# Kernel optimization log

Measured on AMD Instinct MI355X. Metric: run time of the kernel, lower is better.

The kernel has to match this reference:

```python
import jax, jax.numpy as jnp
import numpy as np

NUM_GRAPHS = 256
NEG_SLOPE = 0.2


def _gatv2(x, src, dst, Wl, Wr, att, bias, num_nodes):
    # GATv2Conv (heads=1): e_ij = att . leaky_relu(Wl x_j + Wr x_i), softmax over in-edges of i
    xl = x @ Wl  # [N, H] source transform
    xr = x @ Wr  # [N, H] target transform
    msg = xl[src]                      # [E, H]
    e = jax.nn.leaky_relu(msg + xr[dst], NEG_SLOPE) @ att  # [E]
    # segment softmax over destination node
    e_max = jax.ops.segment_max(e, dst, num_segments=num_nodes)
    e_exp = jnp.exp(e - e_max[dst])
    denom = jax.ops.segment_sum(e_exp, dst, num_segments=num_nodes)
    alpha = e_exp / denom[dst]         # [E]
    out = jax.ops.segment_sum(alpha[:, None] * msg, dst, num_segments=num_nodes)
    return out + bias


def setup_inputs() -> dict:
    key = jax.random.key(0)
    ks = jax.random.split(key, 16)
    N, E, D, H, O = 100000, 1600000, 64, 64, 64
    s = 0.05
    inp = {
        "x": jax.random.normal(ks[0], (N, D), dtype=jnp.float32),
        "edge_index": jax.random.randint(ks[1], (2, E), 0, N, dtype=jnp.int64),
        "batch": jnp.sort(jax.random.randint(ks[2], (N,), 0, NUM_GRAPHS, dtype=jnp.int64)),
        "W1l": jax.random.normal(ks[3], (D, H), dtype=jnp.float32) * s,
        "W1r": jax.random.normal(ks[4], (D, H), dtype=jnp.float32) * s,
        "att1": jax.random.normal(ks[5], (H,), dtype=jnp.float32) * s,
        "b1": jnp.zeros((H,), dtype=jnp.float32),
        "W2": jax.random.normal(ks[6], (H, H), dtype=jnp.float32) * s,
        "att2": jax.random.normal(ks[7], (H,), dtype=jnp.float32) * s,
        "b2": jnp.zeros((H,), dtype=jnp.float32),
        "W3": jax.random.normal(ks[8], (H, H), dtype=jnp.float32) * s,
        "att3": jax.random.normal(ks[9], (H,), dtype=jnp.float32) * s,
        "b3": jnp.zeros((H,), dtype=jnp.float32),
        "Wlin": jax.random.normal(ks[10], (H, O), dtype=jnp.float32) * s,
        "blin": jnp.zeros((O,), dtype=jnp.float32),
    }
    return inp


def reference(x, edge_index, batch, W1l, W1r, att1, b1, W2, att2, b2, W3, att3, b3, Wlin, blin):
    N = x.shape[0]
    # PyG GATv2Conv default add_self_loops=True
    loops = jnp.arange(N, dtype=edge_index.dtype)
    src = jnp.concatenate([edge_index[0], loops])
    dst = jnp.concatenate([edge_index[1], loops])

    h = jax.nn.relu(_gatv2(x, src, dst, W1l, W1r, att1, b1, N))
    h = jax.nn.relu(_gatv2(h, src, dst, W2, W2, att2, b2, N))  # share_weights=True
    h = _gatv2(h, src, dst, W3, W3, att3, b3, N)

    # global mean pool over graphs
    sums = jax.ops.segment_sum(h, batch, num_segments=NUM_GRAPHS)
    cnts = jax.ops.segment_sum(jnp.ones((N,), dtype=h.dtype), batch, num_segments=NUM_GRAPHS)
    pooled = sums / jnp.maximum(cnts, 1.0)[:, None]
    # dropout is identity in eval mode
    return pooled @ Wlin + blin
```

## Files before the change

### kernel.cpp

```cpp
#include <hip/hip_runtime.h>
#include <hip/hip_fp16.h>
#include <math.h>

#define NEG_SLOPE 0.2f
#define NUM_GRAPHS 256
#define LOG2E_F 1.44269504088896f

#define EPB   6656
#define EPT   13
#define BCAP  5120
#define MAXB  392

typedef _Float16 half8 __attribute__((ext_vector_type(8)));
typedef _Float16 f16x2 __attribute__((ext_vector_type(2)));
typedef float f32x4 __attribute__((ext_vector_type(4)));
typedef unsigned u32x4 __attribute__((ext_vector_type(4)));

__device__ __forceinline__ half8 bch8(uint4 u) { return __builtin_bit_cast(half8, u); }
__device__ __forceinline__ f16x2 bc2(unsigned u) { return __builtin_bit_cast(f16x2, u); }

__device__ __forceinline__ float hsum8_bcast(float x) {
    x += __int_as_float(__builtin_amdgcn_update_dpp(0, __float_as_int(x), 0x111, 0xF, 0xF, false));
    x += __int_as_float(__builtin_amdgcn_update_dpp(0, __float_as_int(x), 0x112, 0xF, 0xF, false));
    x += __int_as_float(__builtin_amdgcn_update_dpp(0, __float_as_int(x), 0x114, 0xF, 0xF, false));
    return __int_as_float(__builtin_amdgcn_ds_swizzle(__float_as_int(x), 0xF8));
}


__device__ __forceinline__ void bucketA_body(char* smem, int bid, int t,
                                             const int* __restrict__ src,
                                             const int* __restrict__ dst,
                                             unsigned* __restrict__ bucketFill,
                                             uint2* __restrict__ bucketArr,
                                             int E, int NBUCK) {
    uint2* sEdge = (uint2*)smem;
    unsigned* hist  = (unsigned*)(smem + EPB * 8);
    unsigned* lscan = hist + MAXB;
    unsigned* ebase = lscan + MAXB;
    unsigned* efill = ebase + MAXB;
    int e0 = bid * EPB;
    int cntE = E - e0; if (cntE > EPB) cntE = EPB;

    for (int b = t; b < MAXB; b += 512) { hist[b] = 0u; efill[b] = 0u; }
    __syncthreads();

    int es[EPT], ed[EPT];
#pragma unroll
    for (int k = 0; k < EPT; ++k) {
        int i = t + k * 512;
        bool v = i < cntE;
        es[k] = v ? src[e0 + i] : 0;
        ed[k] = v ? dst[e0 + i] : -1;
        if (v) atomicAdd(&hist[(unsigned)ed[k] >> 8], 1u);
    }
    __syncthreads();

    if (t < 64) {
        unsigned vals[7]; unsigned tot = 0u;
#pragma unroll
        for (int k = 0; k < 7; ++k) {
            int b = t * 7 + k;
            vals[k] = (b < MAXB) ? hist[b] : 0u;
            tot += vals[k];
        }
        unsigned sc = tot;
#pragma unroll
        for (int off = 1; off < 64; off <<= 1) {
            unsigned n = __shfl_up(sc, off, 64);
            if (t >= off) sc += n;
        }
        unsigned run = sc - tot;
#pragma unroll
        for (int k = 0; k < 7; ++k) {
            int b = t * 7 + k;
            if (b < MAXB) { lscan[b] = run; run += vals[k]; }
        }
    }
    __syncthreads();

    for (int b = t; b < NBUCK; b += 512) {
        unsigned c = hist[b];
        ebase[b] = c ? atomicAdd(&bucketFill[b], c) : 0u;
    }
    __syncthreads();

#pragma unroll
    for (int k = 0; k < EPT; ++k) {
        if (ed[k] >= 0) {
            unsigned b = (unsigned)ed[k] >> 8;
            unsigned p = lscan[b] + atomicAdd(&efill[b], 1u);
            sEdge[p] = make_uint2((unsigned)es[k], (unsigned)ed[k]);
        }
    }
    __syncthreads();

    for (int i = t; i < cntE; i += 512) {
        uint2 e = sEdge[i];
        unsigned b = e.y >> 8;
        unsigned pos = ebase[b] + ((unsigned)i - lscan[b]);
        if (pos < BCAP) bucketArr[(size_t)b * BCAP + pos] = e;
    }
}


__device__ __forceinline__ void stage_x32_row(const float* __restrict__ X, _Float16* sXp,
                                              int r0, int lr, int c0, int N) {
    int row = r0 + lr;
    float4 x0, x1, x2, x3;
    if (row < N) {
        const float4* Xv = (const float4*)(X + (size_t)row * 64 + c0);
        x0 = Xv[0]; x1 = Xv[1]; x2 = Xv[2]; x3 = Xv[3];
    } else {
        x0 = x1 = x2 = x3 = make_float4(0.f, 0.f, 0.f, 0.f);
    }
    __half2 hh[8] = {
        __floats2half2_rn(x0.x, x0.y), __floats2half2_rn(x0.z, x0.w),
        __floats2half2_rn(x1.x, x1.y), __floats2half2_rn(x1.z, x1.w),
        __floats2half2_rn(x2.x, x2.y), __floats2half2_rn(x2.z, x2.w),
        __floats2half2_rn(x3.x, x3.y), __floats2half2_rn(x3.z, x3.w)};
    *(uint4*)(sXp + lr * 72 + c0)     = ((uint4*)hh)[0];
    *(uint4*)(sXp + lr * 72 + c0 + 8) = ((uint4*)hh)[1];
}

__device__ __forceinline__ void stage_x16(const __half* __restrict__ X, _Float16* sXp,
                                          int r0, int t, int N) {
    int lr = t >> 2, c0 = (t & 3) * 16;
    int row = r0 + lr;
    uint4 u0 = make_uint4(0u,0u,0u,0u), u1 = u0;
    if (row < N) {
        const uint4* Xv = (const uint4*)(X + (size_t)row * 64 + c0);
        u0 = Xv[0]; u1 = Xv[1];
    }
    *(uint4*)(sXp + lr * 72 + c0)     = u0;
    *(uint4*)(sXp + lr * 72 + c0 + 8) = u1;
}

__device__ __forceinline__ void stage_wt(const float* __restrict__ W, _Float16* sWt, int t) {
    int k = t >> 2, nq = (t & 3) * 16;
    const float4* wr = (const float4*)(W + k * 64 + nq);
    float4 w0 = wr[0], w1 = wr[1], w2 = wr[2], w3 = wr[3];
    float ws[16] = {w0.x, w0.y, w0.z, w0.w, w1.x, w1.y, w1.z, w1.w,
                    w2.x, w2.y, w2.z, w2.w, w3.x, w3.y, w3.z, w3.w};
#pragma unroll
    for (int i = 0; i < 16; ++i)
        sWt[(nq + i) * 72 + k] = (_Float16)ws[i];
}

__device__ __forceinline__ void stage_wt512(const float* __restrict__ W, _Float16* sWt, int t) {
    int k = t >> 3, nq = (t & 7) * 8;
    const float4* wr = (const float4*)(W + k * 64 + nq);
    float4 w0 = wr[0], w1 = wr[1];
    float ws[8] = {w0.x, w0.y, w0.z, w0.w, w1.x, w1.y, w1.z, w1.w};
#pragma unroll
    for (int i = 0; i < 8; ++i)
        sWt[(nq + i) * 72 + k] = (_Float16)ws[i];
}

__device__ __forceinline__ void mfma_tile(const _Float16* sXp, const _Float16* sWt,
                                          int m0, int lane, f32x4 acc[4]) {
    int lrow = lane & 15, hi = lane >> 4;
    uint4 ua0 = *(const uint4*)(sXp + (m0 + lrow) * 72 + hi * 8);
    uint4 ua1 = *(const uint4*)(sXp + (m0 + lrow) * 72 + 32 + hi * 8);
    half8 a0 = bch8(ua0), a1 = bch8(ua1);
#pragma unroll
    for (int nt = 0; nt < 4; ++nt) {
        uint4 ub0 = *(const uint4*)(sWt + (nt * 16 + lrow) * 72 + hi * 8);
        uint4 ub1 = *(const uint4*)(sWt + (nt * 16 + lrow) * 72 + 32 + hi * 8);
        acc[nt] = __builtin_amdgcn_mfma_f32_16x16x32_f16(a0, bch8(ub0), acc[nt], 0, 0, 0);
        acc[nt] = __builtin_amdgcn_mfma_f32_16x16x32_f16(a1, bch8(ub1), acc[nt], 0, 0, 0);
    }
}

__device__ __forceinline__ void mfma_store_co(const f32x4 acc[4], __half* Y16,
                                              _Float16* srow, int r0, int m0,
                                              int lane, int N) {
    int lrow = lane & 15, hi = lane >> 4;
#pragma unroll
    for (int nt = 0; nt < 4; ++nt)
#pragma unroll
        for (int r = 0; r < 4; ++r)
            srow[(hi * 4 + r) * 72 + nt * 16 + lrow] = (_Float16)acc[nt][r];
    __syncthreads();
    int row = lane >> 3, c8 = (lane & 7) * 8;
#pragma unroll
    for (int i = 0; i < 2; ++i) {
        int m = r0 + m0 + row + i * 8;
        uint4 v = *(const uint4*)(srow + (row + i * 8) * 72 + c8);
        if (m < N) *(uint4*)(Y16 + (size_t)m * 64 + c8) = v;
    }
}

__global__ __launch_bounds__(512) void k_gemm1_bucketA(
        const float* __restrict__ X, const float* __restrict__ Wl, const float* __restrict__ Wr,
        __half* __restrict__ Yl16, __half* __restrict__ Yr16, int N,
        const int* __restrict__ src, const int* __restrict__ dst,
        unsigned* __restrict__ bucketFill, uint2* __restrict__ bucketArr,
        int E, int NBUCK, int aBlocks, int g1Blocks,
        const float* __restrict__ att1, const float* __restrict__ att2,
        const float* __restrict__ att3, __half* __restrict__ att16) {
    __shared__ uint4 smemq[3720];
    char* smem = (char*)smemq;
    int bid = blockIdx.x;
    int t = threadIdx.x;
    if (bid < aBlocks) {
        bucketA_body(smem, bid, t, src, dst, bucketFill, bucketArr, E, NBUCK);
        return;
    }
    if (bid >= aBlocks + g1Blocks) {
        if (t < 192) {
            int layer = t >> 6, f = t & 63;
            const float* ap = (layer == 0) ? att1 : (layer == 1) ? att2 : att3;
            att16[layer * 64 + f] = __float2half(ap[f] * LOG2E_F);
        }
        return;
    }
    _Float16* sXp  = (_Float16*)smem;
    _Float16* sWtl = sXp + 128 * 72;
    _Float16* sWtr = sWtl + 64 * 72;
    _Float16* srep = sWtr + 64 * 72;
    int r0 = (bid - aBlocks) * 128;
    stage_x32_row(X, sXp, r0, t >> 2, (t & 3) * 16, N);
    stage_wt512(Wl, sWtl, t);
    stage_wt512(Wr, sWtr, t);
    __syncthreads();
    int lane = t & 63;
    int m0 = (t >> 6) * 16;
    _Float16* srow = srep + (t >> 6) * 16 * 72;
    f32x4 accl[4] = {}, accr[4] = {};
    mfma_tile(sXp, sWtl, m0, lane, accl);
    mfma_tile(sXp, sWtr, m0, lane, accr);
    mfma_store_co(accl, Yl16, srow, r0, m0, lane, N);
    mfma_store_co(accr, Yr16, srow, r0, m0, lane, N);
}

__global__ __launch_bounds__(512) void k_bucketB(const uint2* __restrict__ bucketArr,
                                                 const unsigned* __restrict__ bucketFill,
                                                 int* __restrict__ cnt, int* __restrict__ csrF,
                                                 const int* __restrict__ batch,
                                                 int* __restrict__ gstart,
                                                 int N, int E) {
    __shared__ int stage[256 * 64];
    __shared__ unsigned h[256];
    int t = threadIdx.x;
    int b = blockIdx.x;
    int n0 = b << 8;
    if (t < 256) h[t] = 1u;
    {
        uint4* sz = (uint4*)stage;
#pragma unroll
        for (int k = 0; k < 8; ++k) sz[t + k * 512] = make_uint4(0u, 0u, 0u, 0u);
    }
    __syncthreads();
    if (t < 256) stage[t << 6] = n0 + t;
    __syncthreads();

    unsigned ec = bucketFill[b]; if (ec > BCAP) ec = BCAP;
    for (unsigned i = t; i < ec; i += 512) {
        uint2 e = bucketArr[(size_t)b * BCAP + i];
        unsigned v = e.y & 255u;
        unsigned r = atomicAdd(&h[v], 1u);
        if (r < 64u) {
            unsigned pos = (r < 32u) ? (((r & 7u) << 2) + (r >> 3))
                                     : (32u + ((r & 7u) << 2) + ((r >> 3) - 4u));
            stage[(v << 6) + pos] = (int)e.x;
        }
    }
    __syncthreads();

    int node = n0 + t;
    if (t < 256 && node < N) {
        unsigned d = h[t];
        cnt[node] = (int)(d < 64u ? d : 64u);
        int bb = batch[node];
        if (node == 0) {
            for (int g = 0; g <= bb; ++g) gstart[g] = 0;
        } else {
            int pb = batch[node - 1];
            for (int g = pb + 1; g <= bb; ++g) gstart[g] = node;
        }
        if (node == N - 1) {
            for (int g = bb + 1; g <= NUM_GRAPHS; ++g) gstart[g] = N;
        }
    }

    int nrows = N - n0; if (nrows > 256) nrows = 256;
    int total4 = nrows << 4;
    uint4* d4 = (uint4*)(csrF + ((size_t)n0 << 6));
    const uint4* s4 = (const uint4*)stage;
    for (int k = t; k < total4; k += 512) d4[k] = s4[k];
}

__global__ __launch_bounds__(256) void k_gemm_l2(const __half* __restrict__ X,
                                                 const float* __restrict__ W,
                                                 __half* __restrict__ Y16, int N) {
    __shared__ _Float16 s[64 * 72 + 64 * 72 + 4 * 16 * 72];
    _Float16* sXp = s;
    _Float16* sWt = s + 64 * 72;
    _Float16* srep = sWt + 64 * 72;
    int t = threadIdx.x;
    int r0 = blockIdx.x * 64;
    stage_x16(X, sXp, r0, t, N);
    stage_wt(W, sWt, t);
    __syncthreads();
    int lane = t & 63;
    int m0 = (t >> 6) * 16;
    _Float16* srow = srep + (t >> 6) * 16 * 72;
    f32x4 acc[4] = {};
    mfma_tile(sXp, sWt, m0, lane, acc);
    mfma_store_co(acc, Y16, srow, r0, m0, lane, N);
}


#define AGG_STEP(P, K)                                                       \
    { half8 v_ = bch8(P);                                                    \
      half8 t_ = v_ + X8;                                                    \
      t_ = __builtin_elementwise_max(t_, t_ * (_Float16)NEG_SLOPE);          \
      uint4 tu_ = __builtin_bit_cast(uint4, t_);                             \
      float sc_ = __builtin_amdgcn_fdot2(bc2(ua.x), bc2(tu_.x), 0.f, false); \
      sc_ = __builtin_amdgcn_fdot2(bc2(ua.y), bc2(tu_.y), sc_, false);       \
      sc_ = __builtin_amdgcn_fdot2(bc2(ua.z), bc2(tu_.z), sc_, false);       \
      sc_ = __builtin_amdgcn_fdot2(bc2(ua.w), bc2(tu_.w), sc_, false);       \
      sc_ = hsum8_bcast(sc_);                                                \
      float w_ = ((K) * 8 + s < degs) ? exp2f(sc_) : 0.f;                    \
      l_acc += w_;                                                           \
      _Pragma("unroll") for (int j_ = 0; j_ < 8; ++j_)                       \
          acc[j_] = fmaf((float)v_[j_], w_, acc[j_]);                        \
    }

__global__ void k_agg8(const __half* __restrict__ xl, const __half* __restrict__ xrh,
                       const __half* __restrict__ att16, const float* __restrict__ bias,
                       const int* __restrict__ cnt, const int* __restrict__ csrF,
                       __half* __restrict__ out16, int N, int do_relu) {
    int wid = (blockIdx.x * blockDim.x + threadIdx.x) >> 6;
    if (wid >= N) return;
    int lane = threadIdx.x & 63;
    int q = lane & 7, s = lane >> 3;
    int fb = q * 8;

    int degs = __builtin_amdgcn_readfirstlane(cnt[wid]);
    const int* crow = csrF + ((size_t)wid << 6);

    u32x4 idxv = __builtin_nontemporal_load((const u32x4*)(crow + s * 4));
    uint4 ux = *(const uint4*)(xrh + ((size_t)wid << 6) + fb);
    uint4 ua = *(const uint4*)(att16 + fb);

    uint4 pA = *(const uint4*)(xl + ((size_t)idxv[0] << 6) + fb);
    uint4 pB = *(const uint4*)(xl + ((size_t)idxv[1] << 6) + fb);
    uint4 pC = *(const uint4*)(xl + ((size_t)idxv[2] << 6) + fb);
    uint4 pD = *(const uint4*)(xl + ((size_t)idxv[3] << 6) + fb);

    half8 X8 = bch8(ux);
    float l_acc = 0.f;
    float acc[8];
#pragma unroll
    for (int j = 0; j < 8; ++j) acc[j] = 0.f;

    AGG_STEP(pA, 0);
    if (degs > 8)  AGG_STEP(pB, 1);
    if (degs > 16) AGG_STEP(pC, 2);
    if (degs > 24) {
        AGG_STEP(pD, 3);
        if (degs > 32) {
            u32x4 idx2 = __builtin_nontemporal_load((const u32x4*)(crow + 32 + s * 4));
            uint4 qA = *(const uint4*)(xl + ((size_t)idx2[0] << 6) + fb);
            uint4 qB = *(const uint4*)(xl + ((size_t)idx2[1] << 6) + fb);
            uint4 qC = *(const uint4*)(xl + ((size_t)idx2[2] << 6) + fb);
            uint4 qD = *(const uint4*)(xl + ((size_t)idx2[3] << 6) + fb);
            AGG_STEP(qA, 4);
            if (degs > 40) AGG_STEP(qB, 5);
            if (degs > 48) AGG_STEP(qC, 6);
            if (degs > 56) AGG_STEP(qD, 7);
        }
    }

    l_acc += __shfl_xor(l_acc, 8, 64);
#pragma unroll
    for (int j = 0; j < 8; ++j) acc[j] += __shfl_xor(acc[j], 8, 64);
    int par = s & 1;
    float b0 = par ? acc[4] : acc[0];
    float b1 = par ? acc[5] : acc[1];
    float b2 = par ? acc[6] : acc[2];
    float b3 = par ? acc[7] : acc[3];
#pragma unroll
    for (int o = 16; o <= 32; o <<= 1) {
        l_acc += __shfl_xor(l_acc, o, 64);
        b0 += __shfl_xor(b0, o, 64);
        b1 += __shfl_xor(b1, o, 64);
        b2 += __shfl_xor(b2, o, 64);
        b3 += __shfl_xor(b3, o, 64);
    }

    if (s < 2) {
        float rl = 1.0f / l_acc;
        int fo = fb + s * 4;
        float4 bv = *(const float4*)(bias + fo);
        float a0 = b0 * rl + bv.x;
        float a1 = b1 * rl + bv.y;
        float a2 = b2 * rl + bv.z;
        float a3 = b3 * rl + bv.w;
        if (do_relu) {
            a0 = fmaxf(a0, 0.f); a1 = fmaxf(a1, 0.f);
            a2 = fmaxf(a2, 0.f); a3 = fmaxf(a3, 0.f);
        }
        __half2 h0 = __floats2half2_rn(a0, a1);
        __half2 h1 = __floats2half2_rn(a2, a3);
        uint2 u;
        u.x = __builtin_bit_cast(unsigned, h0);
        u.y = __builtin_bit_cast(unsigned, h1);
        *(uint2*)(out16 + (size_t)wid * 64 + fo) = u;
    }
}


__global__ __launch_bounds__(256) void k_pool_final(const __half* __restrict__ h16,
                                                    const int* __restrict__ gstart,
                                                    const float* __restrict__ Wlin,
                                                    const float* __restrict__ blin,
                                                    float* __restrict__ out) {
    __shared__ float red[4][64];
    int g = blockIdx.x;
    int t = threadIdx.x;
    int w = t >> 6, lane = t & 63;
    int i0 = gstart[g], i1 = gstart[g + 1];
    const unsigned* hu = (const unsigned*)h16;
    int half_ = lane >> 5;
    int u = lane & 31;
    float sx = 0.f, sy = 0.f;
    for (int i = i0 + w * 2 + half_; i < i1; i += 8) {
        unsigned v = hu[(size_t)i * 32 + u];
        float2 p = __half22float2(__builtin_bit_cast(__half2, v));
        sx += p.x; sy += p.y;
    }
    sx += __shfl_xor(sx, 32, 64);
    sy += __shfl_xor(sy, 32, 64);
    if (lane < 32) { red[w][2 * u] = sx; red[w][2 * u + 1] = sy; }
    __syncthreads();
    if (w == 0) {
        float s = red[0][lane] + red[1][lane] + red[2][lane] + red[3][lane];
        float cden = (float)((i1 - i0) > 1 ? (i1 - i0) : 1);
        float pld = s / cden;
        float acc = blin[lane];
        for (int k = 0; k < 64; ++k) {
            acc += __shfl(pld, k, 64) * Wlin[k * 64 + lane];
        }
        out[g * 64 + lane] = acc;
    }
}


extern "C" void kernel_launch(void* const* d_in, const int* in_sizes, int n_in,
                              void* d_out, int out_size, void* d_ws, size_t ws_size,
                              hipStream_t stream) {
    const float* x    = (const float*)d_in[0];
    const int*   ei   = (const int*)d_in[1];
    const int*   batch= (const int*)d_in[2];
    const float* W1l  = (const float*)d_in[3];
    const float* W1r  = (const float*)d_in[4];
    const float* att1 = (const float*)d_in[5];
    const float* b1   = (const float*)d_in[6];
    const float* W2   = (const float*)d_in[7];
    const float* att2 = (const float*)d_in[8];
    const float* b2   = (const float*)d_in[9];
    const float* W3   = (const float*)d_in[10];
    const float* att3 = (const float*)d_in[11];
    const float* b3   = (const float*)d_in[12];
    const float* Wlin = (const float*)d_in[13];
    const float* blin = (const float*)d_in[14];

    const int N = in_sizes[0] / 64;
    const int E = in_sizes[1] / 2;
    const int* src = ei;
    const int* dst = ei + E;
    const int NBUCK = (N + 255) >> 8;

    char* p = (char*)d_ws;
    auto alloc = [&](size_t bytes) -> void* {
        void* r = (void*)p;
        p += (bytes + 255) & ~(size_t)255;
        return r;
    };
    float*  bufB32 = (float*)alloc((size_t)N * 64 * 4);
    __half* buf16  = (__half*)alloc((size_t)N * 64 * 2);
    __half* bufC16 = (__half*)alloc((size_t)N * 64 * 2);
    int*    csrF   = (int*)alloc((size_t)N * 64 * 4);
    int*    cnt    = (int*)alloc((size_t)N * 4);
    int*    gstart = (int*)alloc((size_t)(NUM_GRAPHS + 1) * 4);
    __half* att16  = (__half*)alloc((size_t)3 * 64 * 2);
    uint2*    bucketArr  = (uint2*)bufB32;
    unsigned* bucketFill = (unsigned*)((char*)bufB32 + ((size_t)20 << 20));

    const int B = 256;
    const int gemmBlocks = (N + 63) / 64;
    const int aggBlocks = ((size_t)N * 64 + B - 1) / B;
    const int aBlocks = (E + EPB - 1) / EPB;
    const int g1Blocks = (N + 127) >> 7;

    hipMemsetAsync(bucketFill, 0, (size_t)NBUCK * 4, stream);
    k_gemm1_bucketA<<<aBlocks + g1Blocks + 1, 512, 0, stream>>>(
        x, W1l, W1r, buf16, bufC16, N, src, dst, bucketFill, bucketArr,
        E, NBUCK, aBlocks, g1Blocks, att1, att2, att3, att16);
    k_bucketB<<<NBUCK, 512, 0, stream>>>(bucketArr, bucketFill, cnt, csrF, batch, gstart, N, E);

    k_agg8<<<aggBlocks, B, 0, stream>>>(buf16, bufC16, att16, b1, cnt, csrF,
                                        bufC16, N, 1);
    k_gemm_l2<<<gemmBlocks, B, 0, stream>>>(bufC16, W2, buf16, N);
    k_agg8<<<aggBlocks, B, 0, stream>>>(buf16, buf16, att16 + 64, b2, cnt, csrF,
                                        bufC16, N, 1);
    k_gemm_l2<<<gemmBlocks, B, 0, stream>>>(bufC16, W3, buf16, N);
    k_agg8<<<aggBlocks, B, 0, stream>>>(buf16, buf16, att16 + 128, b3, cnt, csrF,
                                        bufC16, N, 0);

    k_pool_final<<<NUM_GRAPHS, B, 0, stream>>>(bufC16, gstart, Wlin, blin, (float*)d_out);
}
```

Measured before the change: 288.7 us.

## Process two nodes per wave in aggregation, prefetching second node's gathers

The aggregation kernel now assigns two destination nodes (i and i+N/2) to each wavefront. While the first node's attention steps run, the second node's CSR indices and target features are loaded early. Its first neighbour rows are gathered before the first node's reduction and store, hiding gather latency behind the first node's work. The cost is half as many waves, more live registers, and a serialised second pass per wave, which can lower occupancy.

```diff
diff --git a/kernel.cpp b/kernel.cpp
--- a/kernel.cpp
+++ b/kernel.cpp
@@ -327,34 +327,10 @@
           acc[j_] = fmaf((float)v_[j_], w_, acc[j_]);                        \
     }
 
-__global__ void k_agg8(const __half* __restrict__ xl, const __half* __restrict__ xrh,
-                       const __half* __restrict__ att16, const float* __restrict__ bias,
-                       const int* __restrict__ cnt, const int* __restrict__ csrF,
-                       __half* __restrict__ out16, int N, int do_relu) {
-    int wid = (blockIdx.x * blockDim.x + threadIdx.x) >> 6;
-    if (wid >= N) return;
-    int lane = threadIdx.x & 63;
-    int q = lane & 7, s = lane >> 3;
-    int fb = q * 8;
-
-    int degs = __builtin_amdgcn_readfirstlane(cnt[wid]);
-    const int* crow = csrF + ((size_t)wid << 6);
-
-    u32x4 idxv = __builtin_nontemporal_load((const u32x4*)(crow + s * 4));
-    uint4 ux = *(const uint4*)(xrh + ((size_t)wid << 6) + fb);
-    uint4 ua = *(const uint4*)(att16 + fb);
-
-    uint4 pA = *(const uint4*)(xl + ((size_t)idxv[0] << 6) + fb);
-    uint4 pB = *(const uint4*)(xl + ((size_t)idxv[1] << 6) + fb);
-    uint4 pC = *(const uint4*)(xl + ((size_t)idxv[2] << 6) + fb);
-    uint4 pD = *(const uint4*)(xl + ((size_t)idxv[3] << 6) + fb);
-
-    half8 X8 = bch8(ux);
-    float l_acc = 0.f;
-    float acc[8];
-#pragma unroll
-    for (int j = 0; j < 8; ++j) acc[j] = 0.f;
-
+__device__ __forceinline__ void agg_steps(int degs, const int* __restrict__ crow,
+        uint4 pA, uint4 pB, uint4 pC, uint4 pD, half8 X8, uint4 ua,
+        int s, int fb, const __half* __restrict__ xl,
+        float acc[8], float& l_acc) {
     AGG_STEP(pA, 0);
     if (degs > 8)  AGG_STEP(pB, 1);
     if (degs > 16) AGG_STEP(pC, 2);
@@ -372,7 +348,11 @@
             if (degs > 56) AGG_STEP(qD, 7);
         }
     }
-
+}
+
+__device__ __forceinline__ void agg_finish(float acc[8], float l_acc, int s, int fb,
+        const float* __restrict__ bias, __half* __restrict__ out16,
+        int wid, int do_relu) {
     l_acc += __shfl_xor(l_acc, 8, 64);
 #pragma unroll
     for (int j = 0; j < 8; ++j) acc[j] += __shfl_xor(acc[j], 8, 64);
@@ -389,7 +369,6 @@
         b2 += __shfl_xor(b2, o, 64);
         b3 += __shfl_xor(b3, o, 64);
     }
-
     if (s < 2) {
         float rl = 1.0f / l_acc;
         int fo = fb + s * 4;
@@ -408,6 +387,67 @@
         u.x = __builtin_bit_cast(unsigned, h0);
         u.y = __builtin_bit_cast(unsigned, h1);
         *(uint2*)(out16 + (size_t)wid * 64 + fo) = u;
+    }
+}
+
+__global__ __launch_bounds__(256) void k_agg8(
+        const __half* __restrict__ xl, const __half* __restrict__ xrh,
+        const __half* __restrict__ att16, const float* __restrict__ bias,
+        const int* __restrict__ cnt, const int* __restrict__ csrF,
+        __half* __restrict__ out16, int N, int halfN, int do_relu) {
+    int wv = (blockIdx.x * blockDim.x + threadIdx.x) >> 6;
+    if (wv >= halfN) return;
+    int lane = threadIdx.x & 63;
+    int q = lane & 7, s = lane >> 3;
+    int fb = q * 8;
+
+    int widA = wv;
+    int widB = wv + halfN;
+    bool hasB = widB < N;
+
+    int degsA = __builtin_amdgcn_readfirstlane(cnt[widA]);
+    const int* crowA = csrF + ((size_t)widA << 6);
+    u32x4 idxA = __builtin_nontemporal_load((const u32x4*)(crowA + s * 4));
+    uint4 uxA = *(const uint4*)(xrh + ((size_t)widA << 6) + fb);
+    uint4 ua  = *(const uint4*)(att16 + fb);
+
+    uint4 pA = *(const uint4*)(xl + ((size_t)idxA[0] << 6) + fb);
+    uint4 pB = *(const uint4*)(xl + ((size_t)idxA[1] << 6) + fb);
+    uint4 pC = *(const uint4*)(xl + ((size_t)idxA[2] << 6) + fb);
+    uint4 pD = *(const uint4*)(xl + ((size_t)idxA[3] << 6) + fb);
+
+    int degsB = 0;
+    const int* crowB = csrF + ((size_t)widB << 6);
+    u32x4 idxB = {0u, 0u, 0u, 0u};
+    uint4 uxB = make_uint4(0u, 0u, 0u, 0u);
+    if (hasB) {
+        degsB = __builtin_amdgcn_readfirstlane(cnt[widB]);
+        idxB = __builtin_nontemporal_load((const u32x4*)(crowB + s * 4));
+        uxB = *(const uint4*)(xrh + ((size_t)widB << 6) + fb);
+    }
+
+    float acc[8];
+#pragma unroll
+    for (int j = 0; j < 8; ++j) acc[j] = 0.f;
+    float l_acc = 0.f;
+
+    agg_steps(degsA, crowA, pA, pB, pC, pD, bch8(uxA), ua, s, fb, xl, acc, l_acc);
+
+    if (hasB) {
+        pA = *(const uint4*)(xl + ((size_t)idxB[0] << 6) + fb);
+        pB = *(const uint4*)(xl + ((size_t)idxB[1] << 6) + fb);
+        pC = *(const uint4*)(xl + ((size_t)idxB[2] << 6) + fb);
+        pD = *(const uint4*)(xl + ((size_t)idxB[3] << 6) + fb);
+    }
+
+    agg_finish(acc, l_acc, s, fb, bias, out16, widA, do_relu);
+
+    if (hasB) {
+#pragma unroll
+        for (int j = 0; j < 8; ++j) acc[j] = 0.f;
+        l_acc = 0.f;
+        agg_steps(degsB, crowB, pA, pB, pC, pD, bch8(uxB), ua, s, fb, xl, acc, l_acc);
+        agg_finish(acc, l_acc, s, fb, bias, out16, widB, do_relu);
     }
 }
 
@@ -472,6 +512,7 @@
     const int* src = ei;
     const int* dst = ei + E;
     const int NBUCK = (N + 255) >> 8;
+    const int halfN = (N + 1) >> 1;
 
     char* p = (char*)d_ws;
     auto alloc = [&](size_t bytes) -> void* {
@@ -491,7 +532,7 @@
 
     const int B = 256;
     const int gemmBlocks = (N + 63) / 64;
-    const int aggBlocks = ((size_t)N * 64 + B - 1) / B;
+    const int aggBlocks = ((size_t)halfN * 64 + B - 1) / B;
     const int aBlocks = (E + EPB - 1) / EPB;
     const int g1Blocks = (N + 127) >> 7;
 
@@ -502,13 +543,13 @@
     k_bucketB<<<NBUCK, 512, 0, stream>>>(bucketArr, bucketFill, cnt, csrF, batch, gstart, N, E);
 
     k_agg8<<<aggBlocks, B, 0, stream>>>(buf16, bufC16, att16, b1, cnt, csrF,
-                                        bufC16, N, 1);
+                                        bufC16, N, halfN, 1);
     k_gemm_l2<<<gemmBlocks, B, 0, stream>>>(bufC16, W2, buf16, N);
     k_agg8<<<aggBlocks, B, 0, stream>>>(buf16, buf16, att16 + 64, b2, cnt, csrF,
-                                        bufC16, N, 1);
+                                        bufC16, N, halfN, 1);
     k_gemm_l2<<<gemmBlocks, B, 0, stream>>>(bufC16, W3, buf16, N);
     k_agg8<<<aggBlocks, B, 0, stream>>>(buf16, buf16, att16 + 128, b3, cnt, csrF,
-                                        bufC16, N, 0);
+                                        bufC16, N, halfN, 0);
 
     k_pool_final<<<NUM_GRAPHS, B, 0, stream>>>(bufC16, gstart, Wlin, blin, (float*)d_out);
 }
```

New measurement: 292.4 us. Within noise of the previous version (+1.3%).
